# Optimization experiments

Measured on AMD Instinct MI355X. Metric: run time of the kernel, lower is better.

The kernel has to match this reference:

```python
import jax, jax.numpy as jnp
import numpy as np
from jax import lax

B, C, H, W = 512, 1, 256, 256
NG, NP = 4, 3            # num_glimpses, num_patches
GH, GW, SF = 16, 16, 2   # glimpse size, scaling factor
H_G, H_L = 256, 128
FLAT = 64 * 5 * 5        # 16 -(k4,s2)-> 7 -(k3,s1)-> 5


def setup_inputs() -> dict:
    key = jax.random.key(0)
    ks = jax.random.split(key, 16)
    g = lambda k, shape, s=0.05: (jax.random.normal(k, shape, jnp.float32) * s)
    return {
        "x": jax.random.normal(ks[0], (B, C, H, W), jnp.float32),
        "l_t_prev": jax.random.uniform(ks[1], (B, NG, 2), jnp.float32, -1.0, 1.0),
        "conv1_w": g(ks[2], (32, NG * NP, 4, 4)),
        "conv1_b": jnp.zeros((32,), jnp.float32),
        "conv2_w": g(ks[3], (64, 32, 3, 3)),
        "conv2_b": jnp.zeros((64,), jnp.float32),
        "fc1_w": g(ks[4], (H_G, FLAT)),
        "fc1_b": jnp.zeros((H_G,), jnp.float32),
        "fc2_w": g(ks[5], (H_L, 2 * NG)),
        "fc2_b": jnp.zeros((H_L,), jnp.float32),
        "fc3_w": g(ks[6], (H_G + H_L, H_G)),
        "fc3_b": jnp.zeros((H_G + H_L,), jnp.float32),
        "fc4_w": g(ks[7], (H_G + H_L, H_L)),
        "fc4_b": jnp.zeros((H_G + H_L,), jnp.float32),
    }


def _extract(x, l, gh, gw):
    # denormalize [-1,1] -> top-left pixel coords, trunc-toward-zero like .long()
    Bb, Cc, Hh, Ww = x.shape
    sx = (0.5 * ((l[:, 0] + 1.0) * (Hh - 1)) - gh // 2).astype(jnp.int32)
    sy = (0.5 * ((l[:, 1] + 1.0) * (Ww - 1)) - gw // 2).astype(jnp.int32)
    # keep_glimpse_inside_image == clamp start to [0, H-gh] (fixed patch size)
    sx = jnp.clip(sx, 0, Hh - gh)
    sy = jnp.clip(sy, 0, Ww - gw)
    slice_one = lambda img, a, b: lax.dynamic_slice(img, (0, a, b), (Cc, gh, gw))
    patch = jax.vmap(slice_one)(x, sx, sy)          # [B, C, gh, gw]
    bbox = jnp.stack([sy, sx, sy + gw, sx + gh], axis=-1)  # [start_y,start_x,end_y,end_x]
    return patch, bbox


def _pool_to(p, gh, gw):
    Bb, Cc, h, w = p.shape
    kh, kw = h // gh, w // gw
    return p.reshape(Bb, Cc, gh, kh, gw, kw).mean(axis=(3, 5))


def _foveate(x, l):
    phi, bboxes = [], []
    for j in range(NG):
        gh, gw = GH, GW
        for i in range(NP):
            p, bb = _extract(x, l[:, j, :], gh, gw)
            phi.append(_pool_to(p, GH, GW))  # avg-pool pyramid level back to GHxGW
            bboxes.append(bb)
            gh, gw = int(SF * gh), int(SF * gw)
    phi = jnp.concatenate(phi, axis=1)               # [B, NG*NP*C, GH, GW]
    bboxes = jnp.stack(bboxes, axis=1).astype(jnp.float32)  # [B, NG*NP, 4]
    return phi, bboxes


DN = ('NCHW', 'OIHW', 'NCHW')


def reference(x, l_t_prev, conv1_w, conv1_b, conv2_w, conv2_b,
              fc1_w, fc1_b, fc2_w, fc2_b, fc3_w, fc3_b, fc4_w, fc4_b):
    phi, bboxes = _foveate(x, l_t_prev)
    h = lax.conv_general_dilated(phi, conv1_w, (2, 2), 'VALID', dimension_numbers=DN)
    h = jax.nn.relu(h + conv1_b[None, :, None, None])
    h = lax.conv_general_dilated(h, conv2_w, (1, 1), 'VALID', dimension_numbers=DN)
    h = jax.nn.relu(h + conv2_b[None, :, None, None])
    h = h.reshape(h.shape[0], -1)                    # [B, 1600]
    phi_out = jax.nn.relu(h @ fc1_w.T + fc1_b)       # [B, h_g]
    l_flat = l_t_prev.reshape(l_t_prev.shape[0], -1)  # [B, 2*NG]
    l_out = jax.nn.relu(l_flat @ fc2_w.T + fc2_b)    # [B, h_l]
    what = phi_out @ fc3_w.T + fc3_b
    where = l_out @ fc4_w.T + fc4_b
    g_t = jax.nn.relu(what + where)                  # [B, h_g+h_l]
    return phi_out, g_t, bboxes
```

## Files before the change

### kernel.cpp

```cpp
#include <hip/hip_runtime.h>


#define PHI_OUT_OFF 0
#define GT_OFF      131072
#define BBOX_OFF    327680

#define WS_H2    0
#define WS_PART  819200
#define WS_W2T   1867776
#define WS_W1T   1886208

__global__ __launch_bounds__(256) void repack_kernel(
    const float* __restrict__ c2w,
    const float* __restrict__ c1w,
    float* __restrict__ w2t,
    float* __restrict__ w1t)
{
    int idx = blockIdx.x * 256 + threadIdx.x;
    if (idx < 18432) {
        int oc = idx / 288, r = idx % 288;
        w2t[r * 64 + oc] = c2w[idx];
    }
    int g1 = idx - 18432;
    if (g1 >= 0 && g1 < 6144) {
        int oc = g1 / 192, rem = g1 % 192;
        int ch = rem / 16, kk = rem % 16, ky = kk / 4, kx = kk % 4;
        w1t[(ch * 4 + ky) * 128 + kx * 32 + oc] = c1w[g1];
    }
}

__global__ __launch_bounds__(256) void glimpse_conv_kernel(
    const float* __restrict__ x,
    const float* __restrict__ l,
    const float* __restrict__ w1t,
    const float* __restrict__ c1b,
    const float* __restrict__ w2t,
    const float* __restrict__ c2b,
    float* __restrict__ h2,
    float* __restrict__ bbox)
{
    __shared__ float in_s[12 * 16 * 20];
    __shared__ float h1_s[32 * 7 * 8];
    int b = blockIdx.x, t = threadIdx.x;
    int r = t >> 4, c = t & 15;
    const float* xb = x + (size_t)b * 65536;

    #pragma unroll
    for (int j = 0; j < 4; ++j) {
        float l0 = l[(b * 4 + j) * 2 + 0];
        float l1 = l[(b * 4 + j) * 2 + 1];
        {
            int sx = (int)(0.5f * ((l0 + 1.0f) * 255.0f) - 8.0f);
            int sy = (int)(0.5f * ((l1 + 1.0f) * 255.0f) - 8.0f);
            sx = min(max(sx, 0), 240);
            sy = min(max(sy, 0), 240);
            in_s[((j * 3 + 0) * 16 + r) * 20 + c] = xb[(sx + r) * 256 + sy + c];
        }
        {
            int sx = (int)(0.5f * ((l0 + 1.0f) * 255.0f) - 16.0f);
            int sy = (int)(0.5f * ((l1 + 1.0f) * 255.0f) - 16.0f);
            sx = min(max(sx, 0), 224);
            sy = min(max(sy, 0), 224);
            const float* p = xb + (sx + 2 * r) * 256 + sy + 2 * c;
            float v00 = p[0], v01 = p[1], v10 = p[256], v11 = p[257];
            in_s[((j * 3 + 1) * 16 + r) * 20 + c] =
                ((v00 + v01) + (v10 + v11)) * 0.25f;
        }
        {
            int sx = (int)(0.5f * ((l0 + 1.0f) * 255.0f) - 32.0f);
            int sy = (int)(0.5f * ((l1 + 1.0f) * 255.0f) - 32.0f);
            sx = min(max(sx, 0), 192);
            sy = min(max(sy, 0), 192);
            const float* p = xb + (sx + 4 * r) * 256 + sy + 4 * c;
            float v[16];
            #pragma unroll
            for (int dy = 0; dy < 4; ++dy)
                #pragma unroll
                for (int dx = 0; dx < 4; ++dx)
                    v[dy * 4 + dx] = p[dy * 256 + dx];
            float s0 = (v[0]  + v[1])  + (v[2]  + v[3]);
            float s1 = (v[4]  + v[5])  + (v[6]  + v[7]);
            float s2 = (v[8]  + v[9])  + (v[10] + v[11]);
            float s3 = (v[12] + v[13]) + (v[14] + v[15]);
            in_s[((j * 3 + 2) * 16 + r) * 20 + c] =
                ((s0 + s1) + (s2 + s3)) * 0.0625f;
        }
    }
    if (t < 12) {
        int j = t / 3, i = t % 3;
        int gh = 16 << i, half = gh >> 1;
        float l0 = l[(b * 4 + j) * 2 + 0];
        float l1 = l[(b * 4 + j) * 2 + 1];
        int sx = (int)(0.5f * ((l0 + 1.0f) * 255.0f) - (float)half);
        int sy = (int)(0.5f * ((l1 + 1.0f) * 255.0f) - (float)half);
        sx = min(max(sx, 0), 256 - gh);
        sy = min(max(sy, 0), 256 - gh);
        float4 bbv = make_float4((float)sy, (float)sx,
                                 (float)(sy + gh), (float)(sx + gh));
        *(float4*)(bbox + ((size_t)b * 12 + t) * 4) = bbv;
    }
    __syncthreads();

    if (t < 224) {
        int py = t >> 5, oc = t & 31;
        float a[7] = {0.f,0.f,0.f,0.f,0.f,0.f,0.f};
        for (int ch = 0; ch < 12; ++ch) {
            #pragma unroll
            for (int ky = 0; ky < 4; ++ky) {
                const float* rp = in_s + (ch * 16 + 2 * py + ky) * 20;
                float4 r0 = *(const float4*)(rp);
                float4 r1 = *(const float4*)(rp + 4);
                float4 r2 = *(const float4*)(rp + 8);
                float4 r3 = *(const float4*)(rp + 12);
                float row[16] = {r0.x,r0.y,r0.z,r0.w, r1.x,r1.y,r1.z,r1.w,
                                 r2.x,r2.y,r2.z,r2.w, r3.x,r3.y,r3.z,r3.w};
                const float* wp = w1t + (ch * 4 + ky) * 128 + oc;
                float w0 = wp[0], w1 = wp[32], w2 = wp[64], w3 = wp[96];
                #pragma unroll
                for (int px = 0; px < 7; ++px) {
                    int s2 = 2 * px;
                    a[px] += row[s2]*w0 + row[s2+1]*w1
                           + row[s2+2]*w2 + row[s2+3]*w3;
                }
            }
        }
        float bv = c1b[oc];
        #pragma unroll
        for (int px = 0; px < 7; ++px)
            h1_s[oc * 56 + py * 8 + px] = fmaxf(a[px] + bv, 0.0f);
    }
    __syncthreads();

    for (int idx = t; idx < 320; idx += 256) {
        int py = idx >> 6, oc = idx & 63;
        float a[5] = {0.f,0.f,0.f,0.f,0.f};
        for (int ch = 0; ch < 32; ++ch) {
            #pragma unroll
            for (int ky = 0; ky < 3; ++ky) {
                const float* rp = h1_s + ch * 56 + (py + ky) * 8;
                float4 q0 = *(const float4*)(rp);
                float4 q1 = *(const float4*)(rp + 4);
                float row[8] = {q0.x,q0.y,q0.z,q0.w, q1.x,q1.y,q1.z,q1.w};
                #pragma unroll
                for (int kx = 0; kx < 3; ++kx) {
                    float wv = w2t[(ch * 9 + ky * 3 + kx) * 64 + oc];
                    #pragma unroll
                    for (int px = 0; px < 5; ++px)
                        a[px] += row[px + kx] * wv;
                }
            }
        }
        float bv = c2b[oc];
        float* o = h2 + (size_t)b * 1600 + oc * 25 + py * 5;
        #pragma unroll
        for (int px = 0; px < 5; ++px)
            o[px] = fmaxf(a[px] + bv, 0.0f);
    }
}

__global__ __launch_bounds__(256) void fc1_partial_kernel(
    const float* __restrict__ h2,
    const float* __restrict__ w,
    float* __restrict__ partial)
{
    int bt = blockIdx.x, kc = blockIdx.y, t = threadIdx.x;
    const float4* wp = (const float4*)(w + (size_t)t * 1600 + kc * 200);
    const float*  hb = h2 + (size_t)bt * 8 * 1600 + kc * 200;
    float acc[8] = {0.f,0.f,0.f,0.f,0.f,0.f,0.f,0.f};
    for (int k4 = 0; k4 < 50; ++k4) {
        float4 wv = wp[k4];
        #pragma unroll
        for (int bb = 0; bb < 8; ++bb) {
            float4 iv = *(const float4*)(hb + bb * 1600 + k4 * 4);
            acc[bb] += wv.x*iv.x + wv.y*iv.y + wv.z*iv.z + wv.w*iv.w;
        }
    }
    float* pp = partial + ((size_t)kc * 512 + bt * 8) * 256 + t;
    #pragma unroll
    for (int bb = 0; bb < 8; ++bb) pp[bb * 256] = acc[bb];
}

__global__ __launch_bounds__(384) void fc_tail_kernel(
    const float* __restrict__ partial,
    const float* __restrict__ fc1_b,
    const float* __restrict__ l,
    const float* __restrict__ fc2_w,
    const float* __restrict__ fc2_b,
    const float* __restrict__ fc3_w,
    const float* __restrict__ fc3_b,
    const float* __restrict__ fc4_w,
    const float* __restrict__ fc4_b,
    float* __restrict__ phi_out,
    float* __restrict__ g_t)
{
    __shared__ float ph_s[2 * 256];
    __shared__ float lo_s[2 * 128];
    int bt = blockIdx.x, t = threadIdx.x;

    for (int idx = t; idx < 512; idx += 384) {
        int bb = idx >> 8, ch = idx & 255;
        size_t gidx = ((size_t)(bt * 2 + bb)) * 256 + ch;
        float s = fc1_b[ch];
        #pragma unroll
        for (int kc = 0; kc < 8; ++kc) s += partial[(size_t)kc * 131072 + gidx];
        s = fmaxf(s, 0.0f);
        ph_s[idx] = s;
        phi_out[gidx] = s;
    }
    for (int idx = t; idx < 256; idx += 384) {
        int bb = idx >> 7, ch = idx & 127;
        int b = bt * 2 + bb;
        float a = fc2_b[ch];
        const float* lb = l + b * 8;
        const float* wr = fc2_w + ch * 8;
        #pragma unroll
        for (int m = 0; m < 8; ++m) a += lb[m] * wr[m];
        lo_s[idx] = fmaxf(a, 0.0f);
    }
    __syncthreads();

    float base = fc3_b[t] + fc4_b[t];
    float acc[2] = {base, base};
    const float4* w3 = (const float4*)(fc3_w + (size_t)t * 256);
    for (int k4 = 0; k4 < 64; ++k4) {
        float4 wv = w3[k4];
        #pragma unroll
        for (int bb = 0; bb < 2; ++bb) {
            float4 iv = *(const float4*)&ph_s[bb * 256 + k4 * 4];
            acc[bb] += wv.x*iv.x + wv.y*iv.y + wv.z*iv.z + wv.w*iv.w;
        }
    }
    const float4* w4 = (const float4*)(fc4_w + (size_t)t * 128);
    for (int k4 = 0; k4 < 32; ++k4) {
        float4 wv = w4[k4];
        #pragma unroll
        for (int bb = 0; bb < 2; ++bb) {
            float4 iv = *(const float4*)&lo_s[bb * 128 + k4 * 4];
            acc[bb] += wv.x*iv.x + wv.y*iv.y + wv.z*iv.z + wv.w*iv.w;
        }
    }
    #pragma unroll
    for (int bb = 0; bb < 2; ++bb)
        g_t[((size_t)bt * 2 + bb) * 384 + t] = fmaxf(acc[bb], 0.0f);
}

extern "C" void kernel_launch(void* const* d_in, const int* in_sizes, int n_in,
                              void* d_out, int out_size, void* d_ws, size_t ws_size,
                              hipStream_t stream) {
    const float* x   = (const float*)d_in[0];
    const float* l   = (const float*)d_in[1];
    const float* c1w = (const float*)d_in[2];
    const float* c1b = (const float*)d_in[3];
    const float* c2w = (const float*)d_in[4];
    const float* c2b = (const float*)d_in[5];
    const float* f1w = (const float*)d_in[6];
    const float* f1b = (const float*)d_in[7];
    const float* f2w = (const float*)d_in[8];
    const float* f2b = (const float*)d_in[9];
    const float* f3w = (const float*)d_in[10];
    const float* f3b = (const float*)d_in[11];
    const float* f4w = (const float*)d_in[12];
    const float* f4b = (const float*)d_in[13];

    float* out       = (float*)d_out;
    float* phi_out_p = out + PHI_OUT_OFF;
    float* gt_p      = out + GT_OFF;
    float* bbox_p    = out + BBOX_OFF;

    float* ws      = (float*)d_ws;
    float* h2      = ws + WS_H2;
    float* partial = ws + WS_PART;
    float* w2t     = ws + WS_W2T;
    float* w1t     = ws + WS_W1T;

    repack_kernel<<<96, 256, 0, stream>>>(c2w, c1w, w2t, w1t);
    glimpse_conv_kernel<<<512, 256, 0, stream>>>(x, l, w1t, c1b, w2t, c2b,
                                                 h2, bbox_p);
    fc1_partial_kernel<<<dim3(64, 8), 256, 0, stream>>>(h2, f1w, partial);
    fc_tail_kernel<<<256, 384, 0, stream>>>(partial, f1b, l, f2w, f2b,
                                            f3w, f3b, f4w, f4b,
                                            phi_out_p, gt_p);
}
```

Baseline: 80.93 us.

## Stage conv2 weights in double-buffered LDS and transpose fc3/fc4 weights for coalescing

```diff
diff --git a/kernel.cpp b/kernel.cpp
--- a/kernel.cpp
+++ b/kernel.cpp
@@ -9,27 +9,40 @@
 #define WS_PART  819200
 #define WS_W2T   1867776
 #define WS_W1T   1886208
+#define WS_W3T   1892352
+#define WS_W4T   1990656
 
 __global__ __launch_bounds__(256) void repack_kernel(
     const float* __restrict__ c2w,
     const float* __restrict__ c1w,
+    const float* __restrict__ f3w,
+    const float* __restrict__ f4w,
     float* __restrict__ w2t,
-    float* __restrict__ w1t)
+    float* __restrict__ w1t,
+    float* __restrict__ w3t,
+    float* __restrict__ w4t)
 {
     int idx = blockIdx.x * 256 + threadIdx.x;
     if (idx < 18432) {
         int oc = idx / 288, r = idx % 288;
         w2t[r * 64 + oc] = c2w[idx];
-    }
-    int g1 = idx - 18432;
-    if (g1 >= 0 && g1 < 6144) {
+    } else if (idx < 24576) {
+        int g1 = idx - 18432;
         int oc = g1 / 192, rem = g1 % 192;
         int ch = rem / 16, kk = rem % 16, ky = kk / 4, kx = kk % 4;
         w1t[(ch * 4 + ky) * 128 + kx * 32 + oc] = c1w[g1];
-    }
-}
-
-__global__ __launch_bounds__(256) void glimpse_conv_kernel(
+    } else if (idx < 122880) {
+        int i = idx - 24576;
+        int ch = i >> 8, k = i & 255;
+        w3t[((k >> 2) * 384 + ch) * 4 + (k & 3)] = f3w[i];
+    } else if (idx < 172032) {
+        int i = idx - 122880;
+        int ch = i >> 7, k = i & 127;
+        w4t[((k >> 2) * 384 + ch) * 4 + (k & 3)] = f4w[i];
+    }
+}
+
+__global__ __launch_bounds__(320) void glimpse_conv_kernel(
     const float* __restrict__ x,
     const float* __restrict__ l,
     const float* __restrict__ w1t,
@@ -39,51 +52,55 @@
     float* __restrict__ h2,
     float* __restrict__ bbox)
 {
-    __shared__ float in_s[12 * 16 * 20];
-    __shared__ float h1_s[32 * 7 * 8];
+    __shared__ __align__(16) float w2s[2][4608];
+    __shared__ __align__(16) float h1_s[32 * 7 * 8];
+    float* in_s = w2s[1];
     int b = blockIdx.x, t = threadIdx.x;
-    int r = t >> 4, c = t & 15;
     const float* xb = x + (size_t)b * 65536;
 
-    #pragma unroll
-    for (int j = 0; j < 4; ++j) {
-        float l0 = l[(b * 4 + j) * 2 + 0];
-        float l1 = l[(b * 4 + j) * 2 + 1];
-        {
-            int sx = (int)(0.5f * ((l0 + 1.0f) * 255.0f) - 8.0f);
-            int sy = (int)(0.5f * ((l1 + 1.0f) * 255.0f) - 8.0f);
-            sx = min(max(sx, 0), 240);
-            sy = min(max(sy, 0), 240);
-            in_s[((j * 3 + 0) * 16 + r) * 20 + c] = xb[(sx + r) * 256 + sy + c];
-        }
-        {
-            int sx = (int)(0.5f * ((l0 + 1.0f) * 255.0f) - 16.0f);
-            int sy = (int)(0.5f * ((l1 + 1.0f) * 255.0f) - 16.0f);
-            sx = min(max(sx, 0), 224);
-            sy = min(max(sy, 0), 224);
-            const float* p = xb + (sx + 2 * r) * 256 + sy + 2 * c;
-            float v00 = p[0], v01 = p[1], v10 = p[256], v11 = p[257];
-            in_s[((j * 3 + 1) * 16 + r) * 20 + c] =
-                ((v00 + v01) + (v10 + v11)) * 0.25f;
-        }
-        {
-            int sx = (int)(0.5f * ((l0 + 1.0f) * 255.0f) - 32.0f);
-            int sy = (int)(0.5f * ((l1 + 1.0f) * 255.0f) - 32.0f);
-            sx = min(max(sx, 0), 192);
-            sy = min(max(sy, 0), 192);
-            const float* p = xb + (sx + 4 * r) * 256 + sy + 4 * c;
-            float v[16];
-            #pragma unroll
-            for (int dy = 0; dy < 4; ++dy)
+    if (t < 256) {
+        int r = t >> 4, c = t & 15;
+        #pragma unroll
+        for (int j = 0; j < 4; ++j) {
+            float l0 = l[(b * 4 + j) * 2 + 0];
+            float l1 = l[(b * 4 + j) * 2 + 1];
+            {
+                int sx = (int)(0.5f * ((l0 + 1.0f) * 255.0f) - 8.0f);
+                int sy = (int)(0.5f * ((l1 + 1.0f) * 255.0f) - 8.0f);
+                sx = min(max(sx, 0), 240);
+                sy = min(max(sy, 0), 240);
+                in_s[((j * 3 + 0) * 16 + r) * 20 + c] =
+                    xb[(sx + r) * 256 + sy + c];
+            }
+            {
+                int sx = (int)(0.5f * ((l0 + 1.0f) * 255.0f) - 16.0f);
+                int sy = (int)(0.5f * ((l1 + 1.0f) * 255.0f) - 16.0f);
+                sx = min(max(sx, 0), 224);
+                sy = min(max(sy, 0), 224);
+                const float* p = xb + (sx + 2 * r) * 256 + sy + 2 * c;
+                float v00 = p[0], v01 = p[1], v10 = p[256], v11 = p[257];
+                in_s[((j * 3 + 1) * 16 + r) * 20 + c] =
+                    ((v00 + v01) + (v10 + v11)) * 0.25f;
+            }
+            {
+                int sx = (int)(0.5f * ((l0 + 1.0f) * 255.0f) - 32.0f);
+                int sy = (int)(0.5f * ((l1 + 1.0f) * 255.0f) - 32.0f);
+                sx = min(max(sx, 0), 192);
+                sy = min(max(sy, 0), 192);
+                const float* p = xb + (sx + 4 * r) * 256 + sy + 4 * c;
+                float v[16];
                 #pragma unroll
-                for (int dx = 0; dx < 4; ++dx)
-                    v[dy * 4 + dx] = p[dy * 256 + dx];
-            float s0 = (v[0]  + v[1])  + (v[2]  + v[3]);
-            float s1 = (v[4]  + v[5])  + (v[6]  + v[7]);
-            float s2 = (v[8]  + v[9])  + (v[10] + v[11]);
-            float s3 = (v[12] + v[13]) + (v[14] + v[15]);
-            in_s[((j * 3 + 2) * 16 + r) * 20 + c] =
-                ((s0 + s1) + (s2 + s3)) * 0.0625f;
+                for (int dy = 0; dy < 4; ++dy)
+                    #pragma unroll
+                    for (int dx = 0; dx < 4; ++dx)
+                        v[dy * 4 + dx] = p[dy * 256 + dx];
+                float s0 = (v[0]  + v[1])  + (v[2]  + v[3]);
+                float s1 = (v[4]  + v[5])  + (v[6]  + v[7]);
+                float s2 = (v[8]  + v[9])  + (v[10] + v[11]);
+                float s3 = (v[12] + v[13]) + (v[14] + v[15]);
+                in_s[((j * 3 + 2) * 16 + r) * 20 + c] =
+                    ((s0 + s1) + (s2 + s3)) * 0.0625f;
+            }
         }
     }
     if (t < 12) {
@@ -128,13 +145,24 @@
         #pragma unroll
         for (int px = 0; px < 7; ++px)
             h1_s[oc * 56 + py * 8 + px] = fmaxf(a[px] + bv, 0.0f);
+    } else if (t >= 256) {
+        const float4* src = (const float4*)w2t;
+        float4* dst = (float4*)w2s[0];
+        for (int i = t - 256; i < 1152; i += 64) dst[i] = src[i];
     }
     __syncthreads();
 
-    for (int idx = t; idx < 320; idx += 256) {
-        int py = idx >> 6, oc = idx & 63;
-        float a[5] = {0.f,0.f,0.f,0.f,0.f};
-        for (int ch = 0; ch < 32; ++ch) {
+    int py = t >> 6, oc = t & 63;
+    float a[5] = {0.f,0.f,0.f,0.f,0.f};
+    for (int cc = 0; cc < 4; ++cc) {
+        if (cc < 3) {
+            const float4* src = (const float4*)(w2t + (cc + 1) * 4608);
+            float4* dst = (float4*)w2s[(cc + 1) & 1];
+            for (int i = t; i < 1152; i += 320) dst[i] = src[i];
+        }
+        const float* wb = w2s[cc & 1];
+        for (int ch8 = 0; ch8 < 8; ++ch8) {
+            int ch = cc * 8 + ch8;
             #pragma unroll
             for (int ky = 0; ky < 3; ++ky) {
                 const float* rp = h1_s + ch * 56 + (py + ky) * 8;
@@ -143,19 +171,20 @@
                 float row[8] = {q0.x,q0.y,q0.z,q0.w, q1.x,q1.y,q1.z,q1.w};
                 #pragma unroll
                 for (int kx = 0; kx < 3; ++kx) {
-                    float wv = w2t[(ch * 9 + ky * 3 + kx) * 64 + oc];
+                    float wv = wb[(ch8 * 9 + ky * 3 + kx) * 64 + oc];
                     #pragma unroll
                     for (int px = 0; px < 5; ++px)
                         a[px] += row[px + kx] * wv;
                 }
             }
         }
-        float bv = c2b[oc];
-        float* o = h2 + (size_t)b * 1600 + oc * 25 + py * 5;
-        #pragma unroll
-        for (int px = 0; px < 5; ++px)
-            o[px] = fmaxf(a[px] + bv, 0.0f);
-    }
+        __syncthreads();
+    }
+    float bv = c2b[oc];
+    float* o = h2 + (size_t)b * 1600 + oc * 25 + py * 5;
+    #pragma unroll
+    for (int px = 0; px < 5; ++px)
+        o[px] = fmaxf(a[px] + bv, 0.0f);
 }
 
 __global__ __launch_bounds__(256) void fc1_partial_kernel(
@@ -186,15 +215,15 @@
     const float* __restrict__ l,
     const float* __restrict__ fc2_w,
     const float* __restrict__ fc2_b,
-    const float* __restrict__ fc3_w,
+    const float* __restrict__ w3t,
     const float* __restrict__ fc3_b,
-    const float* __restrict__ fc4_w,
+    const float* __restrict__ w4t,
     const float* __restrict__ fc4_b,
     float* __restrict__ phi_out,
     float* __restrict__ g_t)
 {
-    __shared__ float ph_s[2 * 256];
-    __shared__ float lo_s[2 * 128];
+    __shared__ __align__(16) float ph_s[2 * 256];
+    __shared__ __align__(16) float lo_s[2 * 128];
     int bt = blockIdx.x, t = threadIdx.x;
 
     for (int idx = t; idx < 512; idx += 384) {
@@ -220,28 +249,27 @@
     __syncthreads();
 
     float base = fc3_b[t] + fc4_b[t];
-    float acc[2] = {base, base};
-    const float4* w3 = (const float4*)(fc3_w + (size_t)t * 256);
+    float acc0 = base, acc1 = base;
+    const float4* w3p = (const float4*)w3t + t;
+    #pragma unroll 8
     for (int k4 = 0; k4 < 64; ++k4) {
-        float4 wv = w3[k4];
-        #pragma unroll
-        for (int bb = 0; bb < 2; ++bb) {
-            float4 iv = *(const float4*)&ph_s[bb * 256 + k4 * 4];
-            acc[bb] += wv.x*iv.x + wv.y*iv.y + wv.z*iv.z + wv.w*iv.w;
-        }
-    }
-    const float4* w4 = (const float4*)(fc4_w + (size_t)t * 128);
+        float4 wv = w3p[(size_t)k4 * 384];
+        float4 a0 = *(const float4*)&ph_s[k4 * 4];
+        float4 a1 = *(const float4*)&ph_s[256 + k4 * 4];
+        acc0 += wv.x*a0.x + wv.y*a0.y + wv.z*a0.z + wv.w*a0.w;
+        acc1 += wv.x*a1.x + wv.y*a1.y + wv.z*a1.z + wv.w*a1.w;
+    }
+    const float4* w4p = (const float4*)w4t + t;
+    #pragma unroll 8
     for (int k4 = 0; k4 < 32; ++k4) {
-        float4 wv = w4[k4];
-        #pragma unroll
-        for (int bb = 0; bb < 2; ++bb) {
-            float4 iv = *(const float4*)&lo_s[bb * 128 + k4 * 4];
-            acc[bb] += wv.x*iv.x + wv.y*iv.y + wv.z*iv.z + wv.w*iv.w;
-        }
-    }
-    #pragma unroll
-    for (int bb = 0; bb < 2; ++bb)
-        g_t[((size_t)bt * 2 + bb) * 384 + t] = fmaxf(acc[bb], 0.0f);
+        float4 wv = w4p[(size_t)k4 * 384];
+        float4 a0 = *(const float4*)&lo_s[k4 * 4];
+        float4 a1 = *(const float4*)&lo_s[128 + k4 * 4];
+        acc0 += wv.x*a0.x + wv.y*a0.y + wv.z*a0.z + wv.w*a0.w;
+        acc1 += wv.x*a1.x + wv.y*a1.y + wv.z*a1.z + wv.w*a1.w;
+    }
+    g_t[((size_t)bt * 2 + 0) * 384 + t] = fmaxf(acc0, 0.0f);
+    g_t[((size_t)bt * 2 + 1) * 384 + t] = fmaxf(acc1, 0.0f);
 }
 
 extern "C" void kernel_launch(void* const* d_in, const int* in_sizes, int n_in,
@@ -272,12 +300,15 @@
     float* partial = ws + WS_PART;
     float* w2t     = ws + WS_W2T;
     float* w1t     = ws + WS_W1T;
-
-    repack_kernel<<<96, 256, 0, stream>>>(c2w, c1w, w2t, w1t);
-    glimpse_conv_kernel<<<512, 256, 0, stream>>>(x, l, w1t, c1b, w2t, c2b,
+    float* w3t     = ws + WS_W3T;
+    float* w4t     = ws + WS_W4T;
+
+    repack_kernel<<<672, 256, 0, stream>>>(c2w, c1w, f3w, f4w,
+                                           w2t, w1t, w3t, w4t);
+    glimpse_conv_kernel<<<512, 320, 0, stream>>>(x, l, w1t, c1b, w2t, c2b,
                                                  h2, bbox_p);
     fc1_partial_kernel<<<dim3(64, 8), 256, 0, stream>>>(h2, f1w, partial);
     fc_tail_kernel<<<256, 384, 0, stream>>>(partial, f1b, l, f2w, f2b,
-                                            f3w, f3b, f4w, f4b,
+                                            w3t, f3b, w4t, f4b,
                                             phi_out_p, gt_p);
 }
```

New measurement: 89.59 us. +10.7%, slower.
